# Kernel tuning notes

Measured on AMD Instinct MI355X. Metric: run time of the kernel, lower is better.

## Reference

```python
import jax, jax.numpy as jnp
import numpy as np

T, Z, Y, X = 16, 16, 16, 16
NS, NC = 4, 3
D = NS * NC  # 12 internal (spin*color) components
DIAG = 4.5   # 4 + mass
OUT_PARITY = 0


def _r_masks():
    t = jnp.arange(T).reshape(T, 1, 1, 1, 1)
    z = jnp.arange(Z).reshape(1, Z, 1, 1, 1)
    y = jnp.arange(Y).reshape(1, 1, Y, 1, 1)
    r = (t + z + y + OUT_PARITY) % 2
    r = jnp.broadcast_to(r, (T, Z, Y, X // 2, D))
    return r == 1, r == 0  # fwd mask, bwd mask


def _cmatvec(Kr, Ki, vr, vi):
    # complex (K) @ (v) per site; K: [T,Z,Y,X/2,D,D], v: [T,Z,Y,X/2,D]
    ar = jnp.einsum('tzyxij,tzyxj->tzyxi', Kr, vr) - jnp.einsum('tzyxij,tzyxj->tzyxi', Ki, vi)
    ai = jnp.einsum('tzyxij,tzyxj->tzyxi', Kr, vi) + jnp.einsum('tzyxij,tzyxj->tzyxi', Ki, vr)
    return ar, ai


def setup_inputs() -> dict:
    key = jax.random.key(0)
    ks = jax.random.split(key, 6)
    shp_psi = (T, Z, Y, X // 2, NS, NC)
    shp_K = (4, T, Z, Y, X // 2, D, D)
    return {
        'psi_re': jax.random.normal(ks[0], shp_psi, dtype=jnp.float32),
        'psi_im': jax.random.normal(ks[1], shp_psi, dtype=jnp.float32),
        'K_fwd_re': jax.random.normal(ks[2], shp_K, dtype=jnp.float32),
        'K_fwd_im': jax.random.normal(ks[3], shp_K, dtype=jnp.float32),
        'K_bwd_re': jax.random.normal(ks[4], shp_K, dtype=jnp.float32),
        'K_bwd_im': jax.random.normal(ks[5], shp_K, dtype=jnp.float32),
    }


def reference(psi_re, psi_im, K_fwd_re, K_fwd_im, K_bwd_re, K_bwd_im):
    pr = psi_re.reshape(T, Z, Y, X // 2, D)
    pi = psi_im.reshape(T, Z, Y, X // 2, D)
    mask_f, mask_b = _r_masks()
    out_re = DIAG * pr
    out_im = DIAG * pi
    for mu in range(4):
        ax = mu  # ldim = mu - 5 on a rank-5 tensor == axis mu
        if mu < 3:
            pf_re = jnp.roll(pr, -1, axis=ax); pf_im = jnp.roll(pi, -1, axis=ax)
            pb_re = jnp.roll(pr, 1, axis=ax); pb_im = jnp.roll(pi, 1, axis=ax)
        else:
            # staggered X hop on the half-lattice, selected by parity masks
            pf_re = jnp.where(mask_f, jnp.roll(pr, -1, axis=ax), pr)
            pf_im = jnp.where(mask_f, jnp.roll(pi, -1, axis=ax), pi)
            pb_re = jnp.where(mask_b, jnp.roll(pr, 1, axis=ax), pr)
            pb_im = jnp.where(mask_b, jnp.roll(pi, 1, axis=ax), pi)
        cf_re, cf_im = _cmatvec(K_fwd_re[mu], K_fwd_im[mu], pf_re, pf_im)
        cb_re, cb_im = _cmatvec(K_bwd_re[mu], K_bwd_im[mu], pb_re, pb_im)
        out_re = out_re - 0.5 * (cf_re + cb_re)
        out_im = out_im - 0.5 * (cf_im + cb_im)
    return (out_re.reshape(T, Z, Y, X // 2, NS, NC),
            out_im.reshape(T, Z, Y, X // 2, NS, NC))
```

## Files before the change

### kernel.cpp

```cpp
#include <hip/hip_runtime.h>

#define DD 12
#define NSITES 32768
#define SPB 16
#define THREADS 192
#define DIAG 4.5f
#define VSTRIDE 100
#define MU_STRIDE (NSITES*144)
#define SLOT_BYTES 6144
#define WAVE_RING  (2*SLOT_BYTES)

typedef __attribute__((address_space(3))) unsigned int       lds_u32_t;
typedef __attribute__((address_space(1))) const unsigned int gbl_u32_t;

__device__ __forceinline__ void dma16(const float* gp, unsigned char* lp) {
    __builtin_amdgcn_global_load_lds((gbl_u32_t*)gp, (lds_u32_t*)lp, 16, 0, 0);
}

__device__ __forceinline__ void cdot4(const float4 kr, const float4 ki,
                                      const float4 vr, const float4 vi,
                                      float& sr, float& si) {
    sr = fmaf(kr.x, vr.x, sr); sr = fmaf(-ki.x, vi.x, sr);
    si = fmaf(kr.x, vi.x, si); si = fmaf(ki.x, vr.x, si);
    sr = fmaf(kr.y, vr.y, sr); sr = fmaf(-ki.y, vi.y, sr);
    si = fmaf(kr.y, vi.y, si); si = fmaf(ki.y, vr.y, si);
    sr = fmaf(kr.z, vr.z, sr); sr = fmaf(-ki.z, vi.z, sr);
    si = fmaf(kr.z, vi.z, si); si = fmaf(ki.z, vr.z, si);
    sr = fmaf(kr.w, vr.w, sr); sr = fmaf(-ki.w, vi.w, sr);
    si = fmaf(kr.w, vi.w, si); si = fmaf(ki.w, vr.w, si);
}

__global__ __launch_bounds__(THREADS, 2) void hop_kernel(
    const float* __restrict__ psi_re, const float* __restrict__ psi_im,
    const float* __restrict__ K_fwd_re, const float* __restrict__ K_fwd_im,
    const float* __restrict__ K_bwd_re, const float* __restrict__ K_bwd_im,
    float* __restrict__ out_re, float* __restrict__ out_im)
{
    __shared__ alignas(16) unsigned char kring[3 * WAVE_RING];
    __shared__ alignas(16) float vre[SPB][VSTRIDE];
    __shared__ alignas(16) float vim[SPB][VSTRIDE];

    const int tid   = threadIdx.x;
    const int site0 = blockIdx.x * SPB;
    const int wave  = tid >> 6;
    const int lane  = tid & 63;

    const int jj  = tid % 12;
    const int scb = tid / 12;
    const int cc  = scb & 7;
    const int sb  = scb >> 3;
    const int dt = (cc == 0) - (cc == 1);
    const int dz = (cc == 2) - (cc == 3);
    const int dy = (cc == 4) - (cc == 5);

    float tr[8], ti[8];
    int   dst[8];
    #pragma unroll
    for (int k = 0; k < 8; ++k) {
        const int s  = sb + 2 * k;
        const int sg = site0 + s;
        const int x = sg & 7, y = (sg >> 3) & 15, z = (sg >> 7) & 15, t = (sg >> 11) & 15;
        const int r = (t + z + y) & 1;
        int dx = 0;
        if (cc == 6) dx =  (r == 1);
        if (cc == 7) dx = -(r == 0);
        const int nt = (t + dt) & 15, nz = (z + dz) & 15,
                  ny = (y + dy) & 15, nx = (x + dx) & 7;
        const int n = ((nt * 16 + nz) * 16 + ny) * 8 + nx;
        tr[k]  = psi_re[n * 12 + jj];
        ti[k]  = psi_im[n * 12 + jj];
        dst[k] = s * VSTRIDE + cc * 12 + jj;
    }

    const int s    = scb;
    const int i    = jj;
    const int site = site0 + s;
    const float pr_c = psi_re[site * 12 + i];
    const float pi_c = psi_im[site * 12 + i];

    #pragma unroll
    for (int k = 0; k < 8; ++k) {
        ((float*)vre)[dst[k]] = tr[k];
        ((float*)vim)[dst[k]] = ti[k];
    }
    __syncthreads();

    float o_re = DIAG * pr_c;
    float o_im = DIAG * pi_c;

    unsigned char* wring = kring + wave * WAVE_RING;
    const int gw = site0 * 144 + wave * 768 + lane * 4;

    #define ISSUE(c) do { \
        const float* _kr = (((c) & 1) ? K_bwd_re : K_fwd_re) + ((c) >> 1) * MU_STRIDE + gw; \
        const float* _ki = (((c) & 1) ? K_bwd_im : K_fwd_im) + ((c) >> 1) * MU_STRIDE + gw; \
        unsigned char* _sp = wring + ((c) & 1) * SLOT_BYTES; \
        dma16(_kr,       _sp);                dma16(_ki,       _sp + 3072); \
        dma16(_kr + 256, _sp + 1024);         dma16(_ki + 256, _sp + 3072 + 1024); \
        dma16(_kr + 512, _sp + 2048);         dma16(_ki + 512, _sp + 3072 + 2048); \
    } while (0)

    ISSUE(0);

    #pragma unroll
    for (int c = 0; c < 8; ++c) {
        __builtin_amdgcn_sched_barrier(0);
        if (c < 7) ISSUE(c + 1);
        if (c < 7) asm volatile("s_waitcnt vmcnt(6)" ::: "memory");
        else       asm volatile("s_waitcnt vmcnt(0)" ::: "memory");
        const unsigned char* sp = wring + (c & 1) * SLOT_BYTES;
        const float4* kr4 = (const float4*)(sp + lane * 48);
        const float4* ki4 = (const float4*)(sp + 3072 + lane * 48);
        const float4* v4r = (const float4*)&vre[s][c * 12];
        const float4* v4i = (const float4*)&vim[s][c * 12];
        float sr = 0.f, si = 0.f;
        cdot4(kr4[0], ki4[0], v4r[0], v4i[0], sr, si);
        cdot4(kr4[1], ki4[1], v4r[1], v4i[1], sr, si);
        cdot4(kr4[2], ki4[2], v4r[2], v4i[2], sr, si);
        o_re -= 0.5f * sr;
        o_im -= 0.5f * si;
    }
    #undef ISSUE

    out_re[site * 12 + i] = o_re;
    out_im[site * 12 + i] = o_im;
}

extern "C" void kernel_launch(void* const* d_in, const int* in_sizes, int n_in,
                              void* d_out, int out_size, void* d_ws, size_t ws_size,
                              hipStream_t stream) {
    const float* psi_re   = (const float*)d_in[0];
    const float* psi_im   = (const float*)d_in[1];
    const float* K_fwd_re = (const float*)d_in[2];
    const float* K_fwd_im = (const float*)d_in[3];
    const float* K_bwd_re = (const float*)d_in[4];
    const float* K_bwd_im = (const float*)d_in[5];
    float* out_re = (float*)d_out;
    float* out_im = out_re + (out_size / 2);

    hop_kernel<<<NSITES / SPB, THREADS, 0, stream>>>(
        psi_re, psi_im, K_fwd_re, K_fwd_im, K_bwd_re, K_bwd_im, out_re, out_im);
}
```

Before: 274.5 us.

## Replace LDS DMA ring with register double-buffered direct K loads

Drops the per-wave global_load_lds ring buffer and its manual vmcnt waits. Each thread now loads its own 12-float K rows straight into registers as float4s, alternating between two register sets so the next direction's loads overlap the current complex dot product. The first two loads are issued before the barrier. Removing the LDS ring frees shared memory, and launch bounds rise from 2 to 4 blocks per CU for more occupancy. The trade-offs are higher register pressure and 48-byte-strided per-lane vector loads, which are less neatly coalesced than the old DMA pattern.

```diff
diff --git a/kernel.cpp b/kernel.cpp
--- a/kernel.cpp
+++ b/kernel.cpp
@@ -1,21 +1,11 @@
 #include <hip/hip_runtime.h>
 
-#define DD 12
 #define NSITES 32768
 #define SPB 16
 #define THREADS 192
 #define DIAG 4.5f
 #define VSTRIDE 100
 #define MU_STRIDE (NSITES*144)
-#define SLOT_BYTES 6144
-#define WAVE_RING  (2*SLOT_BYTES)
-
-typedef __attribute__((address_space(3))) unsigned int       lds_u32_t;
-typedef __attribute__((address_space(1))) const unsigned int gbl_u32_t;
-
-__device__ __forceinline__ void dma16(const float* gp, unsigned char* lp) {
-    __builtin_amdgcn_global_load_lds((gbl_u32_t*)gp, (lds_u32_t*)lp, 16, 0, 0);
-}
 
 __device__ __forceinline__ void cdot4(const float4 kr, const float4 ki,
                                       const float4 vr, const float4 vi,
@@ -30,20 +20,17 @@
     si = fmaf(kr.w, vi.w, si); si = fmaf(ki.w, vr.w, si);
 }
 
-__global__ __launch_bounds__(THREADS, 2) void hop_kernel(
+__global__ __launch_bounds__(THREADS, 4) void hop_kernel(
     const float* __restrict__ psi_re, const float* __restrict__ psi_im,
     const float* __restrict__ K_fwd_re, const float* __restrict__ K_fwd_im,
     const float* __restrict__ K_bwd_re, const float* __restrict__ K_bwd_im,
     float* __restrict__ out_re, float* __restrict__ out_im)
 {
-    __shared__ alignas(16) unsigned char kring[3 * WAVE_RING];
     __shared__ alignas(16) float vre[SPB][VSTRIDE];
     __shared__ alignas(16) float vim[SPB][VSTRIDE];
 
     const int tid   = threadIdx.x;
     const int site0 = blockIdx.x * SPB;
-    const int wave  = tid >> 6;
-    const int lane  = tid & 63;
 
     const int jj  = tid % 12;
     const int scb = tid / 12;
@@ -57,8 +44,8 @@
     int   dst[8];
     #pragma unroll
     for (int k = 0; k < 8; ++k) {
-        const int s  = sb + 2 * k;
-        const int sg = site0 + s;
+        const int s2 = sb + 2 * k;
+        const int sg = site0 + s2;
         const int x = sg & 7, y = (sg >> 3) & 15, z = (sg >> 7) & 15, t = (sg >> 11) & 15;
         const int r = (t + z + y) & 1;
         int dx = 0;
@@ -69,61 +56,65 @@
         const int n = ((nt * 16 + nz) * 16 + ny) * 8 + nx;
         tr[k]  = psi_re[n * 12 + jj];
         ti[k]  = psi_im[n * 12 + jj];
-        dst[k] = s * VSTRIDE + cc * 12 + jj;
+        dst[k] = s2 * VSTRIDE + cc * 12 + jj;
     }
 
     const int s    = scb;
-    const int i    = jj;
     const int site = site0 + s;
-    const float pr_c = psi_re[site * 12 + i];
-    const float pi_c = psi_im[site * 12 + i];
+    const float pr_c = psi_re[site * 12 + jj];
+    const float pi_c = psi_im[site * 12 + jj];
 
     #pragma unroll
     for (int k = 0; k < 8; ++k) {
         ((float*)vre)[dst[k]] = tr[k];
         ((float*)vim)[dst[k]] = ti[k];
     }
+
+    const int goff = site0 * 144 + tid * 12;
+
+    float4 a0, a1, a2, a3, a4, a5;
+    float4 b0, b1, b2, b3, b4, b5;
+
+#define LOADC(c, R0, R1, R2, I0, I1, I2) do { \
+    const float* _kr = (((c) & 1) ? K_bwd_re : K_fwd_re) + ((c) >> 1) * MU_STRIDE + goff; \
+    const float* _ki = (((c) & 1) ? K_bwd_im : K_fwd_im) + ((c) >> 1) * MU_STRIDE + goff; \
+    R0 = ((const float4*)_kr)[0]; R1 = ((const float4*)_kr)[1]; R2 = ((const float4*)_kr)[2]; \
+    I0 = ((const float4*)_ki)[0]; I1 = ((const float4*)_ki)[1]; I2 = ((const float4*)_ki)[2]; \
+} while (0)
+
+#define COMPUTE(c, R0, R1, R2, I0, I1, I2) do { \
+    const float4* v4r = (const float4*)&vre[s][(c) * 12]; \
+    const float4* v4i = (const float4*)&vim[s][(c) * 12]; \
+    float sr = 0.f, si = 0.f; \
+    cdot4(R0, I0, v4r[0], v4i[0], sr, si); \
+    cdot4(R1, I1, v4r[1], v4i[1], sr, si); \
+    cdot4(R2, I2, v4r[2], v4i[2], sr, si); \
+    o_re -= 0.5f * sr; \
+    o_im -= 0.5f * si; \
+} while (0)
+
+    LOADC(0, a0, a1, a2, a3, a4, a5);
+    LOADC(1, b0, b1, b2, b3, b4, b5);
+
     __syncthreads();
 
     float o_re = DIAG * pr_c;
     float o_im = DIAG * pi_c;
 
-    unsigned char* wring = kring + wave * WAVE_RING;
-    const int gw = site0 * 144 + wave * 768 + lane * 4;
+    COMPUTE(0, a0, a1, a2, a3, a4, a5);  LOADC(2, a0, a1, a2, a3, a4, a5);
+    COMPUTE(1, b0, b1, b2, b3, b4, b5);  LOADC(3, b0, b1, b2, b3, b4, b5);
+    COMPUTE(2, a0, a1, a2, a3, a4, a5);  LOADC(4, a0, a1, a2, a3, a4, a5);
+    COMPUTE(3, b0, b1, b2, b3, b4, b5);  LOADC(5, b0, b1, b2, b3, b4, b5);
+    COMPUTE(4, a0, a1, a2, a3, a4, a5);  LOADC(6, a0, a1, a2, a3, a4, a5);
+    COMPUTE(5, b0, b1, b2, b3, b4, b5);  LOADC(7, b0, b1, b2, b3, b4, b5);
+    COMPUTE(6, a0, a1, a2, a3, a4, a5);
+    COMPUTE(7, b0, b1, b2, b3, b4, b5);
 
-    #define ISSUE(c) do { \
-        const float* _kr = (((c) & 1) ? K_bwd_re : K_fwd_re) + ((c) >> 1) * MU_STRIDE + gw; \
-        const float* _ki = (((c) & 1) ? K_bwd_im : K_fwd_im) + ((c) >> 1) * MU_STRIDE + gw; \
-        unsigned char* _sp = wring + ((c) & 1) * SLOT_BYTES; \
-        dma16(_kr,       _sp);                dma16(_ki,       _sp + 3072); \
-        dma16(_kr + 256, _sp + 1024);         dma16(_ki + 256, _sp + 3072 + 1024); \
-        dma16(_kr + 512, _sp + 2048);         dma16(_ki + 512, _sp + 3072 + 2048); \
-    } while (0)
+#undef LOADC
+#undef COMPUTE
 
-    ISSUE(0);
-
-    #pragma unroll
-    for (int c = 0; c < 8; ++c) {
-        __builtin_amdgcn_sched_barrier(0);
-        if (c < 7) ISSUE(c + 1);
-        if (c < 7) asm volatile("s_waitcnt vmcnt(6)" ::: "memory");
-        else       asm volatile("s_waitcnt vmcnt(0)" ::: "memory");
-        const unsigned char* sp = wring + (c & 1) * SLOT_BYTES;
-        const float4* kr4 = (const float4*)(sp + lane * 48);
-        const float4* ki4 = (const float4*)(sp + 3072 + lane * 48);
-        const float4* v4r = (const float4*)&vre[s][c * 12];
-        const float4* v4i = (const float4*)&vim[s][c * 12];
-        float sr = 0.f, si = 0.f;
-        cdot4(kr4[0], ki4[0], v4r[0], v4i[0], sr, si);
-        cdot4(kr4[1], ki4[1], v4r[1], v4i[1], sr, si);
-        cdot4(kr4[2], ki4[2], v4r[2], v4i[2], sr, si);
-        o_re -= 0.5f * sr;
-        o_im -= 0.5f * si;
-    }
-    #undef ISSUE
-
-    out_re[site * 12 + i] = o_re;
-    out_im[site * 12 + i] = o_im;
+    out_re[site * 12 + jj] = o_re;
+    out_im[site * 12 + jj] = o_im;
 }
 
 extern "C" void kernel_launch(void* const* d_in, const int* in_sizes, int n_in,
```

Result: no change. 279.5 us (+1.8%).
